# Optimization experiments

Hardware: AMD Instinct MI355X
Metric: run time of the kernel (lower is better)

Reference implementation:

```python
import jax, jax.numpy as jnp
import numpy as np

N, E, G = 20000, 320000, 64
F_IN, HID, HEADS, EMB = 32, 64, 4, 64
NEG_SLOPE = 0.2


def _with_self_loops(edge_index, n):
    loop = jnp.arange(n, dtype=edge_index.dtype)
    src = jnp.concatenate([edge_index[0], loop])
    dst = jnp.concatenate([edge_index[1], loop])
    return src, dst


def gat_conv(x, src, dst, W, a_src, a_dst, b, heads, out_ch, n):
    # x:[n,Fin] -> h:[n,H,C]
    h = (x @ W).reshape(n, heads, out_ch)
    al_s = jnp.sum(h * a_src, axis=-1)  # [n,H]
    al_d = jnp.sum(h * a_dst, axis=-1)  # [n,H]
    e = jax.nn.leaky_relu(al_s[src] + al_d[dst], NEG_SLOPE)  # [E',H]
    m = jax.ops.segment_max(e, dst, num_segments=n)
    ex = jnp.exp(e - m[dst])
    denom = jax.ops.segment_sum(ex, dst, num_segments=n)
    alpha = ex / (denom[dst] + 1e-16)  # softmax over incoming edges
    msg = h[src] * alpha[:, :, None]  # [E',H,C]
    out = jax.ops.segment_sum(msg, dst, num_segments=n)  # [n,H,C]
    return out.reshape(n, heads * out_ch) + b


def gcn_conv(x, src, dst, W, b, n):
    deg = jax.ops.segment_sum(jnp.ones_like(src, dtype=x.dtype), dst, num_segments=n)
    dinv = jax.lax.rsqrt(jnp.maximum(deg, 1.0))
    norm = dinv[src] * dinv[dst]  # [E']
    h = x @ W
    out = jax.ops.segment_sum(h[src] * norm[:, None], dst, num_segments=n)
    return out + b


def setup_inputs() -> dict:
    key = jax.random.key(0)
    ks = jax.random.split(key, 24)
    s = 0.05
    inp = {
        'x': jax.random.normal(ks[0], (N, F_IN), dtype=jnp.float32),
        'edge_index': jax.random.randint(ks[1], (2, E), 0, N, dtype=jnp.int32),
        'batch': jnp.sort(jax.random.randint(ks[2], (N,), 0, G, dtype=jnp.int32)),
        # GAT1: 32 -> 64, heads=4
        'W1': jax.random.normal(ks[3], (F_IN, HEADS * HID), dtype=jnp.float32) * s,
        'a_src1': jax.random.normal(ks[4], (HEADS, HID), dtype=jnp.float32) * s,
        'a_dst1': jax.random.normal(ks[5], (HEADS, HID), dtype=jnp.float32) * s,
        'b1': jnp.zeros((HEADS * HID,), dtype=jnp.float32),
        # GAT2: 256 -> 64, heads=1
        'W2': jax.random.normal(ks[6], (HEADS * HID, HID), dtype=jnp.float32) * s,
        'a_src2': jax.random.normal(ks[7], (1, HID), dtype=jnp.float32) * s,
        'a_dst2': jax.random.normal(ks[8], (1, HID), dtype=jnp.float32) * s,
        'b2': jnp.zeros((HID,), dtype=jnp.float32),
        # GCN: 64 -> 32
        'Wg': jax.random.normal(ks[9], (HID, HID // 2), dtype=jnp.float32) * s,
        'bg': jnp.zeros((HID // 2,), dtype=jnp.float32),
        # anomaly head 32->32->16->1
        'A1': jax.random.normal(ks[10], (HID // 2, 32), dtype=jnp.float32) * s,
        'ba1': jnp.zeros((32,), dtype=jnp.float32),
        'A2': jax.random.normal(ks[11], (32, 16), dtype=jnp.float32) * s,
        'ba2': jnp.zeros((16,), dtype=jnp.float32),
        'A3': jax.random.normal(ks[12], (16, 1), dtype=jnp.float32) * s,
        'ba3': jnp.zeros((1,), dtype=jnp.float32),
        # graph embedding 32->64
        'Wemb': jax.random.normal(ks[13], (HID // 2, EMB), dtype=jnp.float32) * s,
        'bemb': jnp.zeros((EMB,), dtype=jnp.float32),
    }
    return inp


def reference(x, edge_index, batch, W1, a_src1, a_dst1, b1, W2, a_src2, a_dst2, b2,
              Wg, bg, A1, ba1, A2, ba2, A3, ba3, Wemb, bemb):
    n = x.shape[0]
    src, dst = _with_self_loops(edge_index, n)
    h = jax.nn.relu(gat_conv(x, src, dst, W1, a_src1, a_dst1, b1, HEADS, HID, n))
    h = jax.nn.relu(gat_conv(h, src, dst, W2, a_src2, a_dst2, b2, 1, HID, n))
    h = jax.nn.relu(gcn_conv(h, src, dst, Wg, bg, n))
    # global mean pool over graph ids
    sums = jax.ops.segment_sum(h, batch, num_segments=G)
    cnts = jax.ops.segment_sum(jnp.ones((n, 1), dtype=h.dtype), batch, num_segments=G)
    pooled = sums / jnp.maximum(cnts, 1.0)  # [G, 32]
    z = jax.nn.relu(pooled @ A1 + ba1)
    z = jax.nn.relu(z @ A2 + ba2)
    anomaly = jax.nn.sigmoid(z @ A3 + ba3)  # [G,1]
    emb = jnp.tanh(pooled @ Wemb + bemb)    # [G,64]
    return (anomaly, emb)
```

## Files before the change

### kernel.cpp

```cpp
#include <hip/hip_runtime.h>
#include <hip/hip_bf16.h>

#define NEG 0.2f

typedef short bf16x8 __attribute__((ext_vector_type(8)));
typedef float floatx4 __attribute__((ext_vector_type(4)));

__device__ __forceinline__ float leaky(float v) { return v > 0.f ? v : NEG * v; }

__device__ __forceinline__ void unpack2(unsigned w, float& lo, float& hi) {
    union { unsigned u; float f; } a, b;
    a.u = w << 16;
    b.u = w & 0xffff0000u;
    lo = a.f; hi = b.f;
}

__device__ __forceinline__ unsigned short f2bf(float f) {
    union { float f; unsigned u; } v; v.f = f;
    unsigned r = v.u + 0x7fff + ((v.u >> 16) & 1);
    return (unsigned short)(r >> 16);
}

__global__ void prelude(const float* __restrict__ x, const float* __restrict__ W1,
                        const float* __restrict__ as1, const float* __restrict__ ad1,
                        const float* __restrict__ W2, const float* __restrict__ Wg,
                        const int* __restrict__ ei,
                        unsigned* __restrict__ xbu,
                        float* __restrict__ als1, float* __restrict__ ald1,
                        unsigned short* __restrict__ W2p,
                        unsigned short* __restrict__ W1p,
                        unsigned short* __restrict__ Wgp,
                        int* __restrict__ deg, int* __restrict__ col64,
                        int n, int E, int nTB, int nFB) {
    __shared__ float xr[64][36];
    __shared__ float WaS[128];
    __shared__ float WaD[128];
    int b = blockIdx.x;
    int t = threadIdx.x;

    if (b >= nTB) {
        int fb = b - nTB;
        if (fb < nFB) {
            int i = fb * 256 + t;
            int tot = E + n;
            if (i < tot) {
                int src, dst;
                if (i < E) { src = ei[i]; dst = ei[E + i]; }
                else { src = i - E; dst = i - E; }
                int slot = atomicAdd(&deg[dst], 1);
                if (slot < 64) col64[(size_t)dst * 64 + slot] = src;
            }
        } else {
            for (int idx = t; idx < 32 * 64; idx += 256) {
                int frag = idx >> 6, lane = idx & 63;
                int ct = frag >> 3, kt = frag & 7;
                int nn = ct * 16 + (lane & 15);
                int kb = kt * 32 + (lane >> 4) * 8;
#pragma unroll
                for (int j = 0; j < 8; j++)
                    W2p[frag * 512 + lane * 8 + j] = f2bf(W2[(kb + j) * 64 + nn]);
            }
            for (int idx = t; idx < 16 * 512; idx += 256) {
                int frag = idx >> 9;
                int h = frag >> 2, nt = frag & 3;
                int pos = idx & 511;
                int lane = pos >> 3, j = pos & 7;
                int coln = lane & 15, quad = lane >> 4;
                int k = quad * 8 + j;
                W1p[idx] = f2bf(W1[k * 256 + h * 64 + nt * 16 + coln]);
            }
            for (int idx = t; idx < 4 * 512; idx += 256) {
                int frag = idx >> 9;
                int nt = frag >> 1, kt = frag & 1;
                int pos = idx & 511;
                int lane = pos >> 3, j = pos & 7;
                int coln = lane & 15, quad = lane >> 4;
                int k = kt * 32 + quad * 8 + j;
                Wgp[idx] = f2bf(Wg[k * 32 + nt * 16 + coln]);
            }
        }
        return;
    }

    int base = b * 64;
    for (int rep = 0; rep < 2; rep++) {
        int s = t + 256 * rep;
        int node = s >> 3, quad = s & 7;
        float4 v = make_float4(0.f, 0.f, 0.f, 0.f);
        if (base + node < n) v = ((const float4*)(x + (size_t)base * 32))[s];
        *((float4*)(&xr[node][quad * 4])) = v;
    }
    {
        int j = (t & 127) >> 2, h = t & 3;
        const float* av = (t < 128) ? as1 : ad1;
        float s_ = 0.f;
#pragma unroll 8
        for (int c = 0; c < 64; c++) s_ += W1[j * 256 + h * 64 + c] * av[h * 64 + c];
        if (t < 128) WaS[t] = s_; else WaD[t - 128] = s_;
    }
    __syncthreads();

    for (int rep = 0; rep < 2; rep++) {
        int q = t + 256 * rep;
        int node = q >> 3, r = q & 7, h = r >> 1, sd = r & 1;
        int gnode = base + node;
        if (gnode < n) {
            const float* cf = sd ? WaD : WaS;
            float d_ = 0.f;
#pragma unroll
            for (int j = 0; j < 32; j++) d_ += xr[node][j] * cf[j * 4 + h];
            if (sd == 0) als1[(size_t)gnode * 4 + h] = d_;
            else         ald1[(size_t)gnode * 4 + h] = d_;
        }
    }
    for (int rep = 0; rep < 4; rep++) {
        int i = t + 256 * rep;
        int node = i >> 4, cp = i & 15;
        int gnode = base + node;
        if (gnode < n) {
            unsigned short u0 = f2bf(xr[node][cp * 2]);
            unsigned short u1 = f2bf(xr[node][cp * 2 + 1]);
            xbu[(size_t)gnode * 16 + cp] = ((unsigned)u1 << 16) | u0;
        }
    }
}

__global__ __launch_bounds__(512) void gat1_agg_mfma(
        const unsigned* __restrict__ xbu,
        const float* __restrict__ als1, const float* __restrict__ ald1,
        const int* __restrict__ deg, const int* __restrict__ col64,
        const float* __restrict__ b1,
        const unsigned short* __restrict__ W1p,
        const unsigned short* __restrict__ W2p,
        const float* __restrict__ asr, const float* __restrict__ adt,
        __hip_bfloat16* __restrict__ h2b,
        float* __restrict__ als, float* __restrict__ ald,
        float* __restrict__ dinv, int n) {
    __shared__ unsigned short xs[16 * 264];
    __shared__ unsigned short agx[16 * 136];
    __shared__ float aps[4][16];
    __shared__ float apd[4][16];
    __shared__ float ewL[8 * 64 * 4];
    __shared__ int   colL[8 * 64];
    int t = threadIdx.x;
    int w = t >> 6, lane = t & 63;
    int base = blockIdx.x * 16;

    {
        int h = lane >> 4, cp = lane & 15;
        for (int rep = 0; rep < 2; rep++) {
            int r = w * 2 + rep;
            int dst = base + r;
            if (dst < n) {
                int dgf = deg[dst];
                int dg = dgf < 64 ? dgf : 64;
                const int* cb = col64 + (size_t)dst * 64;
                {
                    bool v = lane < dg;
                    int s = v ? cb[lane] : 0;
                    float4 as4 = ((const float4*)als1)[s];
                    float4 ad4 = ((const float4*)ald1)[dst];
                    float4 w4;
                    w4.x = v ? __expf(leaky(as4.x + ad4.x)) : 0.f;
                    w4.y = v ? __expf(leaky(as4.y + ad4.y)) : 0.f;
                    w4.z = v ? __expf(leaky(as4.z + ad4.z)) : 0.f;
                    w4.w = v ? __expf(leaky(as4.w + ad4.w)) : 0.f;
                    colL[w * 64 + lane] = s;
                    *((float4*)&ewL[(w * 64 + lane) * 4]) = w4;
                }
                int dgp = (dg + 7) & ~7;
                float a0 = 0.f, a1 = 0.f, ws = 0.f;
                for (int ib = 0; ib < dgp; ib += 8) {
                    int ss[8]; float wv[8];
#pragma unroll
                    for (int u = 0; u < 8; u++) {
                        int i = ib + u;
                        ss[u] = colL[w * 64 + i];
                        wv[u] = ewL[(w * 64 + i) * 4 + h];
                    }
                    float lo[8], hi[8];
#pragma unroll
                    for (int u = 0; u < 8; u++) {
                        unsigned xv = xbu[(size_t)ss[u] * 16 + cp];
                        unpack2(xv, lo[u], hi[u]);
                    }
#pragma unroll
                    for (int u = 0; u < 8; u++) {
                        a0 += lo[u] * wv[u];
                        a1 += hi[u] * wv[u];
                        ws += wv[u];
                    }
                }
                float inv = 1.0f / (ws + 1e-16f);
                unsigned short p0 = f2bf(a0 * inv), p1 = f2bf(a1 * inv);
                *(unsigned*)(agx + r * 136 + h * 32 + cp * 2) =
                    ((unsigned)p1 << 16) | p0;
            } else {
                *(unsigned*)(agx + r * 136 + h * 32 + cp * 2) = 0u;
            }
        }
    }
    __syncthreads();

    if (w < 4) {
        int h = w;
        int mm = lane & 15, quad = lane >> 4;
        bf16x8 a = *((const bf16x8*)(agx + mm * 136 + h * 32 + quad * 8));
#pragma unroll
        for (int nt = 0; nt < 4; nt++) {
            bf16x8 bfr = *((const bf16x8*)(W1p + (h * 4 + nt) * 512 + lane * 8));
            floatx4 c = {0.f, 0.f, 0.f, 0.f};
            c = __builtin_amdgcn_mfma_f32_16x16x32_bf16(a, bfr, c, 0, 0, 0);
            int ch = h * 64 + nt * 16 + mm;
            float bb = b1[ch];
#pragma unroll
            for (int q = 0; q < 4; q++) {
                int node = quad * 4 + q;
                xs[node * 264 + ch] = f2bf(fmaxf(c[q] + bb, 0.f));
            }
        }
    }
    __syncthreads();

    if (w < 4) {
        int m = lane & 15, quad = lane >> 4;
        floatx4 acc = {0.f, 0.f, 0.f, 0.f};
#pragma unroll
        for (int kt = 0; kt < 8; kt++) {
            bf16x8 a = *((const bf16x8*)(xs + m * 264 + kt * 32 + quad * 8));
            bf16x8 b = *((const bf16x8*)(W2p + (w * 8 + kt) * 512 + lane * 8));
            acc = __builtin_amdgcn_mfma_f32_16x16x32_bf16(a, b, acc, 0, 0, 0);
        }
        int colg = w * 16 + m;
        float a_s = asr[colg], a_d = adt[colg];
        float ps[4], pd[4];
#pragma unroll
        for (int q = 0; q < 4; q++) {
            int node = base + quad * 4 + q;
            if (node < n) h2b[(size_t)node * 64 + colg] = __float2bfloat16(acc[q]);
            ps[q] = acc[q] * a_s;
            pd[q] = acc[q] * a_d;
#pragma unroll
            for (int off = 1; off <= 8; off <<= 1) {
                ps[q] += __shfl_xor(ps[q], off);
                pd[q] += __shfl_xor(pd[q], off);
            }
            if (m == 0) {
                aps[w][quad * 4 + q] = ps[q];
                apd[w][quad * 4 + q] = pd[q];
            }
        }
    }
    __syncthreads();
    if (t < 16 && base + t < n) {
        als[base + t] = aps[0][t] + aps[1][t] + aps[2][t] + aps[3][t];
        ald[base + t] = apd[0][t] + apd[1][t] + apd[2][t] + apd[3][t];
        dinv[base + t] = rsqrtf(fmaxf((float)deg[base + t], 1.0f));
    }
}

__global__ __launch_bounds__(512) void gat2_agg_mfma_gcn(
        const unsigned short* __restrict__ h2b,
        const float* __restrict__ als2, const float* __restrict__ ald2,
        const int* __restrict__ deg, const int* __restrict__ col64,
        const float* __restrict__ b2,
        const unsigned short* __restrict__ Wgp,
        unsigned short* __restrict__ h3b, int n) {
    __shared__ unsigned short h2L[16 * 72];
    __shared__ float ewL2[8 * 64];
    __shared__ int   colL2[8 * 64];
    int t = threadIdx.x;
    int w = t >> 6, lane = t & 63;
    int base = blockIdx.x * 16;
    int eg = lane >> 3, cl = lane & 7;

    for (int rep = 0; rep < 2; rep++) {
        int r = w * 2 + rep;
        int dst = base + r;
        if (dst < n) {
            int dgf = deg[dst];
            int dg = dgf < 64 ? dgf : 64;
            const int* cb = col64 + (size_t)dst * 64;
            float a_d = ald2[dst];
            {
                bool v = lane < dg;
                int s = v ? cb[lane] : 0;
                colL2[w * 64 + lane] = s;
                ewL2[w * 64 + lane] = v ? __expf(leaky(als2[s] + a_d)) : 0.f;
            }
            float acc[8];
#pragma unroll
            for (int j = 0; j < 8; j++) acc[j] = 0.f;
            float wsum = 0.f;
            for (int ib = 0; ib < dg; ib += 16) {
                int i0 = ib + eg, i1 = ib + 8 + eg;
                int s0 = colL2[w * 64 + i0], s1 = colL2[w * 64 + i1];
                float w0 = ewL2[w * 64 + i0], w1 = ewL2[w * 64 + i1];
                uint4 hv0 = *((const uint4*)(h2b + (size_t)s0 * 64) + cl);
                uint4 hv1 = *((const uint4*)(h2b + (size_t)s1 * 64) + cl);
                wsum += w0 + w1;
                float l0, u0, l1, u1, l2, u2, l3, u3;
                unpack2(hv0.x, l0, u0); unpack2(hv0.y, l1, u1);
                unpack2(hv0.z, l2, u2); unpack2(hv0.w, l3, u3);
                acc[0] += l0 * w0; acc[1] += u0 * w0;
                acc[2] += l1 * w0; acc[3] += u1 * w0;
                acc[4] += l2 * w0; acc[5] += u2 * w0;
                acc[6] += l3 * w0; acc[7] += u3 * w0;
                unpack2(hv1.x, l0, u0); unpack2(hv1.y, l1, u1);
                unpack2(hv1.z, l2, u2); unpack2(hv1.w, l3, u3);
                acc[0] += l0 * w1; acc[1] += u0 * w1;
                acc[2] += l1 * w1; acc[3] += u1 * w1;
                acc[4] += l2 * w1; acc[5] += u2 * w1;
                acc[6] += l3 * w1; acc[7] += u3 * w1;
            }
#pragma unroll
            for (int off = 8; off <= 32; off <<= 1) {
                wsum += __shfl_xor(wsum, off);
#pragma unroll
                for (int j = 0; j < 8; j++) acc[j] += __shfl_xor(acc[j], off);
            }
            float inv = 1.0f / (wsum + 1e-16f);
            if (lane < 8) {
                const float* bb = b2 + cl * 8;
                unsigned short pk[8];
#pragma unroll
                for (int j = 0; j < 8; j++)
                    pk[j] = f2bf(fmaxf(acc[j] * inv + bb[j], 0.f));
                *((uint4*)(h2L + r * 72 + cl * 8)) = *(const uint4*)pk;
            }
        } else if (lane < 8) {
            unsigned short z[8] = {0, 0, 0, 0, 0, 0, 0, 0};
            *((uint4*)(h2L + r * 72 + cl * 8)) = *(const uint4*)z;
        }
    }
    __syncthreads();

    if (w < 2) {
        int m = lane & 15, quad = lane >> 4;
        floatx4 acc = {0.f, 0.f, 0.f, 0.f};
#pragma unroll
        for (int kt = 0; kt < 2; kt++) {
            bf16x8 a = *((const bf16x8*)(h2L + m * 72 + kt * 32 + quad * 8));
            bf16x8 bfr = *((const bf16x8*)(Wgp + (w * 2 + kt) * 512 + lane * 8));
            acc = __builtin_amdgcn_mfma_f32_16x16x32_bf16(a, bfr, acc, 0, 0, 0);
        }
#pragma unroll
        for (int q = 0; q < 4; q++) {
            int node = base + quad * 4 + q;
            if (node < n) h3b[(size_t)node * 32 + w * 16 + m] = f2bf(acc[q]);
        }
    }
}

__global__ void gcn_agg_pool(const unsigned short* __restrict__ h3b,
                             const float* __restrict__ dinv,
                             const int* __restrict__ deg, const int* __restrict__ col64,
                             const float* __restrict__ bg, const int* __restrict__ batch,
                             float* __restrict__ pooled, int n) {
    __shared__ float rowL[4][32];
    __shared__ int gL[4];
    __shared__ int   colL3[4 * 64];
    __shared__ float nwL3[4 * 64];
    int t = threadIdx.x;
    int w = t >> 6, lane = t & 63;
    int dst = blockIdx.x * 4 + w;
    bool act = dst < n;
    if (act) {
        int dgf = deg[dst];
        int dg = dgf < 64 ? dgf : 64;
        const int* cb = col64 + (size_t)dst * 64;
        float dv = dinv[dst];
        {
            bool v = lane < dg;
            int s = v ? cb[lane] : 0;
            colL3[w * 64 + lane] = s;
            nwL3[w * 64 + lane] = v ? dinv[s] * dv : 0.f;
        }
        int eg = lane >> 3;
        int cl = lane & 7;
        float4 acc = make_float4(0.f, 0.f, 0.f, 0.f);
        for (int ib = 0; ib < dg; ib += 16) {
            int i0 = ib + eg, i1 = ib + 8 + eg;
            int s0 = colL3[w * 64 + i0], s1 = colL3[w * 64 + i1];
            float n0 = nwL3[w * 64 + i0], n1 = nwL3[w * 64 + i1];
            uint2 hv0 = *((const uint2*)(h3b + (size_t)s0 * 32) + cl);
            uint2 hv1 = *((const uint2*)(h3b + (size_t)s1 * 32) + cl);
            float l0, u0, l1, u1;
            unpack2(hv0.x, l0, u0); unpack2(hv0.y, l1, u1);
            acc.x += l0 * n0; acc.y += u0 * n0;
            acc.z += l1 * n0; acc.w += u1 * n0;
            unpack2(hv1.x, l0, u0); unpack2(hv1.y, l1, u1);
            acc.x += l0 * n1; acc.y += u0 * n1;
            acc.z += l1 * n1; acc.w += u1 * n1;
        }
#pragma unroll
        for (int off = 8; off <= 32; off <<= 1) {
            acc.x += __shfl_xor(acc.x, off);
            acc.y += __shfl_xor(acc.y, off);
            acc.z += __shfl_xor(acc.z, off);
            acc.w += __shfl_xor(acc.w, off);
        }
        if (lane == 0) gL[w] = batch[dst];
        if (lane < 8) {
            float4 bb = ((const float4*)bg)[cl];
            float4 o;
            o.x = fmaxf(acc.x + bb.x, 0.f);
            o.y = fmaxf(acc.y + bb.y, 0.f);
            o.z = fmaxf(acc.z + bb.z, 0.f);
            o.w = fmaxf(acc.w + bb.w, 0.f);
            *((float4*)&rowL[w][cl * 4]) = o;
        }
    } else if (lane == 0) {
        gL[w] = -1;
    }
    __syncthreads();
    if (t < 32) {
        float cur = 0.f; int curg = -1;
#pragma unroll
        for (int r = 0; r < 4; r++) {
            int g = gL[r];
            if (g < 0) continue;
            float v = rowL[r][t];
            if (g == curg) cur += v;
            else {
                if (curg >= 0) atomicAdd(&pooled[curg * 32 + t], cur);
                curg = g; cur = v;
            }
        }
        if (curg >= 0) atomicAdd(&pooled[curg * 32 + t], cur);
    }
}

__device__ __forceinline__ int lbound(const int* __restrict__ b, int n, int key) {
    int lo = 0, hi = n;
    while (lo < hi) { int m = (lo + hi) >> 1; if (b[m] < key) lo = m + 1; else hi = m; }
    return lo;
}

__global__ void head_kernel(const float* __restrict__ pooled_s,
                            const int* __restrict__ batch, int n,
                            const float* __restrict__ A1, const float* __restrict__ ba1,
                            const float* __restrict__ A2, const float* __restrict__ ba2,
                            const float* __restrict__ A3, const float* __restrict__ ba3,
                            const float* __restrict__ Wemb, const float* __restrict__ bemb,
                            float* __restrict__ out) {
    __shared__ float P[64 * 32];
    __shared__ float Z1[64 * 32];
    __shared__ float Z2[64 * 16];
    __shared__ int cntL[64];
    int t = threadIdx.x;
    if (t < 64) cntL[t] = lbound(batch, n, t + 1) - lbound(batch, n, t);
    __syncthreads();
    for (int i = t; i < 64 * 32; i += 256) {
        int g = i >> 5;
        P[i] = pooled_s[i] / fmaxf((float)cntL[g], 1.0f);
    }
    __syncthreads();
    for (int i = t; i < 64 * 32; i += 256) {
        int g = i >> 5, c = i & 31;
        float a = ba1[c];
#pragma unroll
        for (int k = 0; k < 32; k++) a += P[g * 32 + k] * A1[k * 32 + c];
        Z1[i] = a > 0.f ? a : 0.f;
    }
    __syncthreads();
    for (int i = t; i < 64 * 16; i += 256) {
        int g = i >> 4, c = i & 15;
        float a = ba2[c];
#pragma unroll
        for (int k = 0; k < 32; k++) a += Z1[g * 32 + k] * A2[k * 16 + c];
        Z2[i] = a > 0.f ? a : 0.f;
    }
    __syncthreads();
    for (int g = t; g < 64; g += 256) {
        float a = ba3[0];
#pragma unroll
        for (int k = 0; k < 16; k++) a += Z2[g * 16 + k] * A3[k];
        out[g] = 1.0f / (1.0f + expf(-a));
    }
    for (int i = t; i < 64 * 64; i += 256) {
        int g = i >> 6, c = i & 63;
        float a = bemb[c];
#pragma unroll
        for (int k = 0; k < 32; k++) a += P[g * 32 + k] * Wemb[k * 64 + c];
        out[64 + i] = tanhf(a);
    }
}

extern "C" void kernel_launch(void* const* d_in, const int* in_sizes, int n_in,
                              void* d_out, int out_size, void* d_ws, size_t ws_size,
                              hipStream_t stream) {
    const float* x    = (const float*)d_in[0];
    const int*   ei   = (const int*)d_in[1];
    const int*   batch= (const int*)d_in[2];
    const float* W1   = (const float*)d_in[3];
    const float* as1  = (const float*)d_in[4];
    const float* ad1  = (const float*)d_in[5];
    const float* b1   = (const float*)d_in[6];
    const float* W2   = (const float*)d_in[7];
    const float* as2  = (const float*)d_in[8];
    const float* ad2  = (const float*)d_in[9];
    const float* b2   = (const float*)d_in[10];
    const float* Wg   = (const float*)d_in[11];
    const float* bg   = (const float*)d_in[12];
    const float* A1   = (const float*)d_in[13];
    const float* ba1  = (const float*)d_in[14];
    const float* A2   = (const float*)d_in[15];
    const float* ba2  = (const float*)d_in[16];
    const float* A3   = (const float*)d_in[17];
    const float* ba3  = (const float*)d_in[18];
    const float* Wemb = (const float*)d_in[19];
    const float* bemb = (const float*)d_in[20];
    float* out = (float*)d_out;

    const int N = in_sizes[0] / 32;
    const int E = in_sizes[1] / 2;
    const int ET = E + N;

    char* base = (char*)d_ws;
    size_t off = 0;
    auto take = [&](size_t bytes) -> char* {
        char* p = base + off;
        off = (off + bytes + 255) & ~(size_t)255;
        return p;
    };
    int*   deg    = (int*)take((size_t)N * 4);
    float* pooled = (float*)take(64 * 32 * 4);
    size_t zspan  = off;
    int*   col64  = (int*)take((size_t)N * 64 * 4);
    float* dinv   = (float*)take((size_t)N * 4);
    float* als1   = (float*)take((size_t)N * 16);
    float* ald1   = (float*)take((size_t)N * 16);
    unsigned short* W2p = (unsigned short*)take(32 * 512 * 2);
    unsigned short* W1p = (unsigned short*)take(16 * 512 * 2);
    unsigned short* Wgp = (unsigned short*)take(4 * 512 * 2);
    unsigned* xbu = (unsigned*)take((size_t)N * 64);
    __hip_bfloat16* h2b = (__hip_bfloat16*)take((size_t)N * 128);
    float* als2 = (float*)take((size_t)N * 4);
    float* ald2 = (float*)take((size_t)N * 4);
    unsigned short* h3b = (unsigned short*)take((size_t)N * 64);

    int gN4 = (N + 3) / 4;
    int gN16 = (N + 15) / 16;
    int gT = (N + 63) / 64;
    int gF = (ET + 255) / 256;
    int gPre = gT + gF + 1;

    hipMemsetAsync(d_ws, 0, zspan, stream);

    prelude<<<gPre, 256, 0, stream>>>(x, W1, as1, ad1, W2, Wg, ei, xbu,
                                      als1, ald1, W2p, W1p, Wgp, deg, col64,
                                      N, E, gT, gF);
    gat1_agg_mfma<<<gN16, 512, 0, stream>>>(xbu, als1, ald1, deg, col64, b1,
                                            W1p, W2p, as2, ad2,
                                            h2b, als2, ald2, dinv, N);
    gat2_agg_mfma_gcn<<<gN16, 512, 0, stream>>>((const unsigned short*)h2b,
                                                als2, ald2, deg, col64, b2,
                                                Wgp, h3b, N);
    gcn_agg_pool<<<gN4, 256, 0, stream>>>(h3b, dinv, deg, col64, bg, batch,
                                          pooled, N);
    head_kernel<<<1, 256, 0, stream>>>(pooled, batch, N, A1, ba1, A2, ba2, A3, ba3,
                                       Wemb, bemb, out);
}
```

Before: 179.4 us.

## Precompute block-wide edge weights and column lists in shared memory before aggregation

Each aggregation kernel now starts with a block-cooperative phase that loads the column indices and computes the attention or normalization weights for all 16 destination rows of the block into shared memory, followed by a barrier. Before, each wave did this per row inside its loop. The GCN pooling kernel now handles 16 nodes per block with 4 rows per wave, which cuts the number of pooled atomics and blocks. The change separates the gather-latency-bound weight computation from the feature accumulation so more independent loads are in flight, at the cost of more shared memory per block and an extra barrier.

```diff
diff --git a/kernel.cpp b/kernel.cpp
--- a/kernel.cpp
+++ b/kernel.cpp
@@ -140,11 +140,35 @@
     __shared__ unsigned short agx[16 * 136];
     __shared__ float aps[4][16];
     __shared__ float apd[4][16];
-    __shared__ float ewL[8 * 64 * 4];
-    __shared__ int   colL[8 * 64];
+    __shared__ float ewL[1024 * 4];
+    __shared__ int   colL[1024];
     int t = threadIdx.x;
     int w = t >> 6, lane = t & 63;
     int base = blockIdx.x * 16;
+
+    for (int rep = 0; rep < 2; rep++) {
+        int idx = t + 512 * rep;
+        int r = idx >> 6, e = idx & 63;
+        int dst = base + r;
+        int s = 0;
+        float4 w4 = make_float4(0.f, 0.f, 0.f, 0.f);
+        if (dst < n) {
+            int dgf = deg[dst];
+            int dg = dgf < 64 ? dgf : 64;
+            if (e < dg) {
+                s = col64[(size_t)dst * 64 + e];
+                float4 as4 = ((const float4*)als1)[s];
+                float4 ad4 = ((const float4*)ald1)[dst];
+                w4.x = __expf(leaky(as4.x + ad4.x));
+                w4.y = __expf(leaky(as4.y + ad4.y));
+                w4.z = __expf(leaky(as4.z + ad4.z));
+                w4.w = __expf(leaky(as4.w + ad4.w));
+            }
+        }
+        colL[idx] = s;
+        *((float4*)&ewL[idx * 4]) = w4;
+    }
+    __syncthreads();
 
     {
         int h = lane >> 4, cp = lane & 15;
@@ -154,29 +178,15 @@
             if (dst < n) {
                 int dgf = deg[dst];
                 int dg = dgf < 64 ? dgf : 64;
-                const int* cb = col64 + (size_t)dst * 64;
-                {
-                    bool v = lane < dg;
-                    int s = v ? cb[lane] : 0;
-                    float4 as4 = ((const float4*)als1)[s];
-                    float4 ad4 = ((const float4*)ald1)[dst];
-                    float4 w4;
-                    w4.x = v ? __expf(leaky(as4.x + ad4.x)) : 0.f;
-                    w4.y = v ? __expf(leaky(as4.y + ad4.y)) : 0.f;
-                    w4.z = v ? __expf(leaky(as4.z + ad4.z)) : 0.f;
-                    w4.w = v ? __expf(leaky(as4.w + ad4.w)) : 0.f;
-                    colL[w * 64 + lane] = s;
-                    *((float4*)&ewL[(w * 64 + lane) * 4]) = w4;
-                }
                 int dgp = (dg + 7) & ~7;
                 float a0 = 0.f, a1 = 0.f, ws = 0.f;
                 for (int ib = 0; ib < dgp; ib += 8) {
                     int ss[8]; float wv[8];
 #pragma unroll
                     for (int u = 0; u < 8; u++) {
-                        int i = ib + u;
-                        ss[u] = colL[w * 64 + i];
-                        wv[u] = ewL[(w * 64 + i) * 4 + h];
+                        int i = r * 64 + ib + u;
+                        ss[u] = colL[i];
+                        wv[u] = ewL[i * 4 + h];
                     }
                     float lo[8], hi[8];
 #pragma unroll
@@ -267,12 +277,30 @@
         const unsigned short* __restrict__ Wgp,
         unsigned short* __restrict__ h3b, int n) {
     __shared__ unsigned short h2L[16 * 72];
-    __shared__ float ewL2[8 * 64];
-    __shared__ int   colL2[8 * 64];
+    __shared__ float ewL2[1024];
+    __shared__ int   colL2[1024];
     int t = threadIdx.x;
     int w = t >> 6, lane = t & 63;
     int base = blockIdx.x * 16;
     int eg = lane >> 3, cl = lane & 7;
+
+    for (int rep = 0; rep < 2; rep++) {
+        int idx = t + 512 * rep;
+        int r = idx >> 6, e = idx & 63;
+        int dst = base + r;
+        int s = 0; float wv = 0.f;
+        if (dst < n) {
+            int dgf = deg[dst];
+            int dg = dgf < 64 ? dgf : 64;
+            if (e < dg) {
+                s = col64[(size_t)dst * 64 + e];
+                wv = __expf(leaky(als2[s] + ald2[dst]));
+            }
+        }
+        colL2[idx] = s;
+        ewL2[idx] = wv;
+    }
+    __syncthreads();
 
     for (int rep = 0; rep < 2; rep++) {
         int r = w * 2 + rep;
@@ -280,22 +308,14 @@
         if (dst < n) {
             int dgf = deg[dst];
             int dg = dgf < 64 ? dgf : 64;
-            const int* cb = col64 + (size_t)dst * 64;
-            float a_d = ald2[dst];
-            {
-                bool v = lane < dg;
-                int s = v ? cb[lane] : 0;
-                colL2[w * 64 + lane] = s;
-                ewL2[w * 64 + lane] = v ? __expf(leaky(als2[s] + a_d)) : 0.f;
-            }
             float acc[8];
 #pragma unroll
             for (int j = 0; j < 8; j++) acc[j] = 0.f;
             float wsum = 0.f;
             for (int ib = 0; ib < dg; ib += 16) {
-                int i0 = ib + eg, i1 = ib + 8 + eg;
-                int s0 = colL2[w * 64 + i0], s1 = colL2[w * 64 + i1];
-                float w0 = ewL2[w * 64 + i0], w1 = ewL2[w * 64 + i1];
+                int i0 = r * 64 + ib + eg, i1 = r * 64 + ib + 8 + eg;
+                int s0 = colL2[i0], s1 = colL2[i1];
+                float w0 = ewL2[i0], w1 = ewL2[i1];
                 uint4 hv0 = *((const uint4*)(h2b + (size_t)s0 * 64) + cl);
                 uint4 hv1 = *((const uint4*)(h2b + (size_t)s1 * 64) + cl);
                 wsum += w0 + w1;
@@ -357,67 +377,80 @@
                              const int* __restrict__ deg, const int* __restrict__ col64,
                              const float* __restrict__ bg, const int* __restrict__ batch,
                              float* __restrict__ pooled, int n) {
-    __shared__ float rowL[4][32];
-    __shared__ int gL[4];
-    __shared__ int   colL3[4 * 64];
-    __shared__ float nwL3[4 * 64];
+    __shared__ float rowL[16][32];
+    __shared__ int gL[16];
+    __shared__ int   colL3[1024];
+    __shared__ float nwL3[1024];
     int t = threadIdx.x;
     int w = t >> 6, lane = t & 63;
-    int dst = blockIdx.x * 4 + w;
-    bool act = dst < n;
-    if (act) {
-        int dgf = deg[dst];
-        int dg = dgf < 64 ? dgf : 64;
-        const int* cb = col64 + (size_t)dst * 64;
-        float dv = dinv[dst];
-        {
-            bool v = lane < dg;
-            int s = v ? cb[lane] : 0;
-            colL3[w * 64 + lane] = s;
-            nwL3[w * 64 + lane] = v ? dinv[s] * dv : 0.f;
-        }
-        int eg = lane >> 3;
-        int cl = lane & 7;
-        float4 acc = make_float4(0.f, 0.f, 0.f, 0.f);
-        for (int ib = 0; ib < dg; ib += 16) {
-            int i0 = ib + eg, i1 = ib + 8 + eg;
-            int s0 = colL3[w * 64 + i0], s1 = colL3[w * 64 + i1];
-            float n0 = nwL3[w * 64 + i0], n1 = nwL3[w * 64 + i1];
-            uint2 hv0 = *((const uint2*)(h3b + (size_t)s0 * 32) + cl);
-            uint2 hv1 = *((const uint2*)(h3b + (size_t)s1 * 32) + cl);
-            float l0, u0, l1, u1;
-            unpack2(hv0.x, l0, u0); unpack2(hv0.y, l1, u1);
-            acc.x += l0 * n0; acc.y += u0 * n0;
-            acc.z += l1 * n0; acc.w += u1 * n0;
-            unpack2(hv1.x, l0, u0); unpack2(hv1.y, l1, u1);
-            acc.x += l0 * n1; acc.y += u0 * n1;
-            acc.z += l1 * n1; acc.w += u1 * n1;
-        }
-#pragma unroll
-        for (int off = 8; off <= 32; off <<= 1) {
-            acc.x += __shfl_xor(acc.x, off);
-            acc.y += __shfl_xor(acc.y, off);
-            acc.z += __shfl_xor(acc.z, off);
-            acc.w += __shfl_xor(acc.w, off);
-        }
-        if (lane == 0) gL[w] = batch[dst];
-        if (lane < 8) {
-            float4 bb = ((const float4*)bg)[cl];
-            float4 o;
-            o.x = fmaxf(acc.x + bb.x, 0.f);
-            o.y = fmaxf(acc.y + bb.y, 0.f);
-            o.z = fmaxf(acc.z + bb.z, 0.f);
-            o.w = fmaxf(acc.w + bb.w, 0.f);
-            *((float4*)&rowL[w][cl * 4]) = o;
-        }
-    } else if (lane == 0) {
-        gL[w] = -1;
+    int base = blockIdx.x * 16;
+
+    for (int rep = 0; rep < 4; rep++) {
+        int idx = t + 256 * rep;
+        int r = idx >> 6, e = idx & 63;
+        int dst = base + r;
+        int s = 0; float nw = 0.f;
+        if (dst < n) {
+            int dgf = deg[dst];
+            int dg = dgf < 64 ? dgf : 64;
+            if (e < dg) {
+                s = col64[(size_t)dst * 64 + e];
+                nw = dinv[s] * dinv[dst];
+            }
+        }
+        colL3[idx] = s;
+        nwL3[idx] = nw;
+    }
+    __syncthreads();
+
+    int eg = lane >> 3, cl = lane & 7;
+    for (int rep = 0; rep < 4; rep++) {
+        int r = w * 4 + rep;
+        int dst = base + r;
+        if (dst < n) {
+            int dgf = deg[dst];
+            int dg = dgf < 64 ? dgf : 64;
+            float4 acc = make_float4(0.f, 0.f, 0.f, 0.f);
+            for (int ib = 0; ib < dg; ib += 16) {
+                int i0 = r * 64 + ib + eg, i1 = r * 64 + ib + 8 + eg;
+                int s0 = colL3[i0], s1 = colL3[i1];
+                float n0 = nwL3[i0], n1 = nwL3[i1];
+                uint2 hv0 = *((const uint2*)(h3b + (size_t)s0 * 32) + cl);
+                uint2 hv1 = *((const uint2*)(h3b + (size_t)s1 * 32) + cl);
+                float l0, u0, l1, u1;
+                unpack2(hv0.x, l0, u0); unpack2(hv0.y, l1, u1);
+                acc.x += l0 * n0; acc.y += u0 * n0;
+                acc.z += l1 * n0; acc.w += u1 * n0;
+                unpack2(hv1.x, l0, u0); unpack2(hv1.y, l1, u1);
+                acc.x += l0 * n1; acc.y += u0 * n1;
+                acc.z += l1 * n1; acc.w += u1 * n1;
+            }
+#pragma unroll
+            for (int off = 8; off <= 32; off <<= 1) {
+                acc.x += __shfl_xor(acc.x, off);
+                acc.y += __shfl_xor(acc.y, off);
+                acc.z += __shfl_xor(acc.z, off);
+                acc.w += __shfl_xor(acc.w, off);
+            }
+            if (lane == 0) gL[r] = batch[dst];
+            if (lane < 8) {
+                float4 bb = ((const float4*)bg)[cl];
+                float4 o;
+                o.x = fmaxf(acc.x + bb.x, 0.f);
+                o.y = fmaxf(acc.y + bb.y, 0.f);
+                o.z = fmaxf(acc.z + bb.z, 0.f);
+                o.w = fmaxf(acc.w + bb.w, 0.f);
+                *((float4*)&rowL[r][cl * 4]) = o;
+            }
+        } else if (lane == 0) {
+            gL[r] = -1;
+        }
     }
     __syncthreads();
     if (t < 32) {
         float cur = 0.f; int curg = -1;
 #pragma unroll
-        for (int r = 0; r < 4; r++) {
+        for (int r = 0; r < 16; r++) {
             int g = gL[r];
             if (g < 0) continue;
             float v = rowL[r][t];
@@ -540,7 +573,6 @@
     float* ald2 = (float*)take((size_t)N * 4);
     unsigned short* h3b = (unsigned short*)take((size_t)N * 64);
 
-    int gN4 = (N + 3) / 4;
     int gN16 = (N + 15) / 16;
     int gT = (N + 63) / 64;
     int gF = (ET + 255) / 256;
@@ -557,8 +589,8 @@
     gat2_agg_mfma_gcn<<<gN16, 512, 0, stream>>>((const unsigned short*)h2b,
                                                 als2, ald2, deg, col64, b2,
                                                 Wgp, h3b, N);
-    gcn_agg_pool<<<gN4, 256, 0, stream>>>(h3b, dinv, deg, col64, bg, batch,
-                                          pooled, N);
+    gcn_agg_pool<<<gN16, 256, 0, stream>>>(h3b, dinv, deg, col64, bg, batch,
+                                           pooled, N);
     head_kernel<<<1, 256, 0, stream>>>(pooled, batch, N, A1, ba1, A2, ba2, A3, ba3,
                                        Wemb, bemb, out);
 }
```

New measurement: 182.0 us. Within noise of the previous version (+1.4%).
